# Optimization experiments

Hardware: AMD Instinct MI355X
Metric: run time of the kernel (lower is better)

Reference implementation:

```python
import jax, jax.numpy as jnp
import numpy as np

B, C, S = 16, 128, 32          # batch, in_channel, img_size
HOLE_LO, HOLE_HI = 8, 24       # 16x16 hole where mask==1
HW = S * S
K = HW - (HOLE_HI - HOLE_LO) ** 2   # 768 context (unmasked) pixels per image
EPS = 1e-8                     # torch CosineSimilarity default eps


def setup_inputs() -> dict:
    key = jax.random.key(0)
    ks = jax.random.split(key, 3)
    x = jax.random.normal(ks[0], (B, C, S, S), dtype=jnp.float32)
    # mask: 1 inside the hole, 0 on the context region (fixed K per batch item)
    mask = jnp.zeros((B, 1, S, S), jnp.float32).at[:, :, HOLE_LO:HOLE_HI, HOLE_LO:HOLE_HI].set(1.0)
    # conv_regular_1: Conv2d(img_size**2 -> 256, k=5, pad=2); conv_regular_2: 256 -> 128
    W1 = jax.random.normal(ks[1], (256, HW, 5, 5), jnp.float32) / np.sqrt(HW * 25)
    b1 = jnp.zeros((256,), jnp.float32)
    W2 = jax.random.normal(ks[2], (128, 256, 5, 5), jnp.float32) / np.sqrt(256 * 25)
    b2 = jnp.zeros((128,), jnp.float32)
    return {"x": x, "mask": mask, "W1": W1, "b1": b1, "W2": W2, "b2": b2}


def _conv5x5(x, w, b):
    y = jax.lax.conv_general_dilated(x, w, window_strides=(1, 1),
                                     padding=[(2, 2), (2, 2)],
                                     dimension_numbers=("NCHW", "OIHW", "NCHW"))
    return y + b[None, :, None, None]


def reference(x, mask, W1, b1, W2, b2):
    # context (unmasked) pixel indices, row-major like torch.masked_select
    inv = (1.0 - mask[:, 0]) > 0.5                       # [B,S,S] bool
    idx = jax.vmap(lambda m: jnp.nonzero(m, size=K, fill_value=0)[0])(inv.reshape(B, HW))  # [B,K]
    xf = x.reshape(B, C, HW)                             # [B,C,HW]
    feat = jnp.take_along_axis(xf, idx[:, None, :], axis=2)  # [B,C,K] context features
    # cosine similarity over channel dim WITHOUT materializing [B,C,K,H,W] repeats
    dot = jnp.einsum("bck,bcp->bkp", feat, xf)           # [B,K,HW]
    nf = jnp.maximum(jnp.sqrt(jnp.sum(feat * feat, axis=1)), EPS)  # [B,K]
    nx = jnp.maximum(jnp.sqrt(jnp.sum(xf * xf, axis=1)), EPS)      # [B,HW]
    out = (dot / (nf[:, :, None] * nx[:, None, :])).reshape(B, K, S, S)
    out = out * mask                                     # keep hole region only
    pad = jnp.zeros((B, HW - K, S, S), out.dtype)
    out = jnp.concatenate([out, pad], axis=1)            # [B, HW, S, S]
    out = jax.nn.elu(_conv5x5(out, W1, b1))              # [B,256,S,S]
    out = jax.nn.elu(_conv5x5(out, W2, b2))              # [B,128,S,S]
    return out
```

## Files before the change

kernel.cpp:

```cpp
#include <hip/hip_runtime.h>
#include <hip/hip_fp16.h>
#include <math.h>


#define CC 128
#define HWN 1024
#define KK 768
#define PH 256

typedef _Float16 f16x8 __attribute__((ext_vector_type(8)));
typedef float f32x4 __attribute__((ext_vector_type(4)));

__device__ __forceinline__ int ctx_p(int k) {
    if (k < 256) return k;
    if (k < 512) {
        int r = (k - 256) >> 4, ci = (k - 256) & 15;
        int c = ci < 8 ? ci : ci + 16;
        return (8 + r) * 32 + c;
    }
    return k + 256;
}

__global__ __launch_bounds__(256) void knorm(const float* __restrict__ x, float* __restrict__ rn) {
    int i = blockIdx.x * 256 + threadIdx.x;
    int b = i >> 10, p = i & 1023;
    const float* xp = x + b * CC * HWN + p;
    float ss = 0.f;
#pragma unroll 8
    for (int c = 0; c < CC; ++c) {
        float v = xp[c * HWN];
        ss = fmaf(v, v, ss);
    }
    rn[i] = 1.0f / fmaxf(sqrtf(ss), 1e-8f);
}

__global__ __launch_bounds__(256) void kcos(const float* __restrict__ x, const float* __restrict__ rn,
                                            _Float16* __restrict__ cosT) {
    __shared__ float f[4][CC];
    __shared__ float rf[4];
    const int b = blockIdx.z, g = blockIdx.y;
    const int t = threadIdx.x;
    const int p4 = g * 4;
    for (int s = t; s < 4 * CC; s += 256) {
        int j = s >> 7, c = s & 127;
        int hp = p4 + j;
        f[j][c] = x[(b * CC + c) * HWN + (8 + (hp >> 4)) * 32 + 8 + (hp & 15)];
    }
    if (t < 4) {
        int hp = p4 + t;
        rf[t] = rn[b * HWN + (8 + (hp >> 4)) * 32 + 8 + (hp & 15)];
    }
    __syncthreads();
    const int k = blockIdx.x * 256 + t;
    const int cp = ctx_p(k);
    const float* xp = x + b * CC * HWN + cp;
    float a0 = 0.f, a1 = 0.f, a2 = 0.f, a3 = 0.f;
#pragma unroll 4
    for (int c = 0; c < CC; ++c) {
        float xv = xp[c * HWN];
        a0 = fmaf(f[0][c], xv, a0);
        a1 = fmaf(f[1][c], xv, a1);
        a2 = fmaf(f[2][c], xv, a2);
        a3 = fmaf(f[3][c], xv, a3);
    }
    const float rk = rn[b * HWN + cp];
    _Float16* o = cosT + ((size_t)(b * PH + p4)) * KK + k;
    o[0]          = (_Float16)(a0 * rf[0] * rk);
    o[KK]         = (_Float16)(a1 * rf[1] * rk);
    o[2 * KK]     = (_Float16)(a2 * rf[2] * rk);
    o[3 * KK]     = (_Float16)(a3 * rf[3] * rk);
}

__global__ __launch_bounds__(256) void kprepW1(const float* __restrict__ W1, _Float16* __restrict__ Wh1) {
    const int oc = blockIdx.y;
    const int k = blockIdx.x * 256 + threadIdx.x;
    const float* wp = W1 + ((size_t)oc * HWN + k) * 25;
#pragma unroll
    for (int tap = 0; tap < 25; ++tap)
        Wh1[((size_t)(tap * 256 + oc)) * KK + k] = (_Float16)wp[tap];
}

__global__ __launch_bounds__(256) void kprepW2(const float* __restrict__ W2, _Float16* __restrict__ Wh2) {
    const int oc = blockIdx.x;
    const int ic = threadIdx.x;
    const float* wp = W2 + ((size_t)oc * 256 + ic) * 25;
#pragma unroll
    for (int tap = 0; tap < 25; ++tap)
        Wh2[((size_t)(tap * 128 + oc)) * 256 + ic] = (_Float16)wp[tap];
}

#define C1_MFMA(mi)                                                                          \
    {                                                                                        \
        int pos = pb[mi] + padd;                                                             \
        f16x8 af = *(const f16x8*)(As + pos * 64 + ((kslot ^ (pos & 3)) << 4));              \
        acc[mi][0] = __builtin_amdgcn_mfma_f32_16x16x32_f16(af, bf0, acc[mi][0], 0, 0, 0);   \
        acc[mi][1] = __builtin_amdgcn_mfma_f32_16x16x32_f16(af, bf1, acc[mi][1], 0, 0, 0);   \
    }

__global__ __launch_bounds__(512) void kconv1m(const _Float16* __restrict__ cosT,
                                               const _Float16* __restrict__ Wh1,
                                               float* __restrict__ P) {
    __shared__ __align__(16) char As[576 * 64];
    const int b = blockIdx.z, nq = blockIdx.y, ks = blockIdx.x;
    const int t = threadIdx.x;
    const int lane = t & 63, wid = t >> 6;
    const int mg = wid >> 1, ng = wid & 1;
    const int lm = lane & 15, kslot = lane >> 4;
    const int mbase = (mg == 0) ? 0 : 1 + 6 * mg;
    int pb[7];
#pragma unroll
    for (int mi = 0; mi < 7; ++mi) {
        int p = (mbase + mi) * 16 + lm;
        if (p > 399) p = 399;
        pb[mi] = (p / 20) * 24 + (p % 20);
    }
    const f32x4 zero = {0.f, 0.f, 0.f, 0.f};
    f32x4 acc[7][2];
#pragma unroll
    for (int mi = 0; mi < 7; ++mi) { acc[mi][0] = zero; acc[mi][1] = zero; }

    const int kbeg = ks * 192;
    for (int kc = kbeg; kc < kbeg + 192; kc += 32) {
        __syncthreads();
        for (int s = t; s < 2304; s += 512) {
            int pos = s >> 2, slot = s & 3;
            int pu = pos / 24, pv = pos - pu * 24;
            int4 val = {0, 0, 0, 0};
            if (pu >= 4 && pu < 20 && pv >= 4 && pv < 20) {
                int hp = (pu - 4) * 16 + (pv - 4);
                val = *(const int4*)(cosT + ((size_t)(b * PH + hp)) * KK + kc + slot * 8);
            }
            *(int4*)(As + pos * 64 + ((slot ^ (pos & 3)) << 4)) = val;
        }
        __syncthreads();
        for (int dy = 0; dy < 5; ++dy) {
            for (int dx = 0; dx < 5; ++dx) {
                const int tap = dy * 5 + dx;
                const f16x8 bf0 = *(const f16x8*)(Wh1 + ((size_t)(tap * 256 + nq * 64 + ng * 32 + lm)) * KK + kc + kslot * 8);
                const f16x8 bf1 = *(const f16x8*)(Wh1 + ((size_t)(tap * 256 + nq * 64 + ng * 32 + 16 + lm)) * KK + kc + kslot * 8);
                const int padd = dy * 24 + dx;
#pragma unroll
                for (int mi = 0; mi < 6; ++mi) C1_MFMA(mi)
                if (mg == 0) C1_MFMA(6)
            }
        }
    }
    float* Ps = P + ((size_t)((ks * 16 + b) * 4 + nq)) * 25600;
#pragma unroll
    for (int mi = 0; mi < 7; ++mi) {
        if (mi == 6 && mg != 0) break;
#pragma unroll
        for (int j = 0; j < 2; ++j)
#pragma unroll
            for (int r = 0; r < 4; ++r) {
                int p = (mbase + mi) * 16 + kslot * 4 + r;
                Ps[p * 64 + ng * 32 + j * 16 + lm] = acc[mi][j][r];
            }
    }
}

__global__ __launch_bounds__(256) void kreduce1(const float* __restrict__ P, const float* __restrict__ b1,
                                                _Float16* __restrict__ Y1T) {
    int i = blockIdx.x * 256 + threadIdx.x;
    int ocl = i & 63;
    int nq = (i >> 6) & 3;
    int bp = i >> 8;
    int p = bp % 400, b = bp / 400;
    float s = 0.f;
#pragma unroll
    for (int ks = 0; ks < 4; ++ks)
        s += P[((size_t)((ks * 16 + b) * 4 + nq)) * 25600 + p * 64 + ocl];
    int oc = nq * 64 + ocl;
    float y = s + b1[oc];
    y = y > 0.f ? y : expm1f(y);
    Y1T[((size_t)(b * 400 + p)) * 256 + oc] = (_Float16)y;
}

__global__ __launch_bounds__(512) void kconv2m(const _Float16* __restrict__ Y1T,
                                               const _Float16* __restrict__ Wh2,
                                               float* __restrict__ P) {
    __shared__ __align__(16) char As[784 * 64];
    const int b = blockIdx.z, mh = blockIdx.y, ks = blockIdx.x;
    const int t = threadIdx.x;
    const int lane = t & 63, wid = t >> 6;
    const int mg = wid >> 2, ng = wid & 3;
    const int lm = lane & 15, kslot = lane >> 4;
    const int ic0 = ks * 32;
    for (int s = t; s < 3136; s += 512) {
        int pos = s >> 2, slot = s & 3;
        int r = pos / 28, c = pos - r * 28;
        int4 val = {0, 0, 0, 0};
        if (r >= 4 && r < 24 && c >= 4 && c < 24)
            val = *(const int4*)(Y1T + ((size_t)(b * 400 + (r - 4) * 20 + (c - 4))) * 256 + ic0 + slot * 8);
        *(int4*)(As + pos * 64 + ((slot ^ (pos & 3)) << 4)) = val;
    }
    int pbs[9];
#pragma unroll
    for (int mi = 0; mi < 9; ++mi) {
        int p = (mh * 18 + mg * 9 + mi) * 16 + lm;
        pbs[mi] = (p / 24) * 28 + (p % 24);
    }
    const f32x4 zero = {0.f, 0.f, 0.f, 0.f};
    f32x4 acc[9][2];
#pragma unroll
    for (int mi = 0; mi < 9; ++mi) { acc[mi][0] = zero; acc[mi][1] = zero; }
    __syncthreads();
    for (int dy = 0; dy < 5; ++dy) {
        for (int dx = 0; dx < 5; ++dx) {
            const int tap = dy * 5 + dx;
            const f16x8 bf0 = *(const f16x8*)(Wh2 + ((size_t)(tap * 128 + ng * 32 + lm)) * 256 + ic0 + kslot * 8);
            const f16x8 bf1 = *(const f16x8*)(Wh2 + ((size_t)(tap * 128 + ng * 32 + 16 + lm)) * 256 + ic0 + kslot * 8);
            const int padd = dy * 28 + dx;
#pragma unroll
            for (int mi = 0; mi < 9; ++mi) {
                int pos = pbs[mi] + padd;
                f16x8 af = *(const f16x8*)(As + pos * 64 + ((kslot ^ (pos & 3)) << 4));
                acc[mi][0] = __builtin_amdgcn_mfma_f32_16x16x32_f16(af, bf0, acc[mi][0], 0, 0, 0);
                acc[mi][1] = __builtin_amdgcn_mfma_f32_16x16x32_f16(af, bf1, acc[mi][1], 0, 0, 0);
            }
        }
    }
    float* Ps = P + ((size_t)((ks * 16 + b) * 2 + mh)) * 36864;
#pragma unroll
    for (int mi = 0; mi < 9; ++mi)
#pragma unroll
        for (int j = 0; j < 2; ++j)
#pragma unroll
            for (int r = 0; r < 4; ++r) {
                int p = (mg * 9 + mi) * 16 + kslot * 4 + r;
                Ps[p * 128 + ng * 32 + j * 16 + lm] = acc[mi][j][r];
            }
}

__global__ __launch_bounds__(256) void kreduce2(const float* __restrict__ P, const float* __restrict__ b2,
                                                float* __restrict__ out) {
    int i = blockIdx.x * 256 + threadIdx.x;
    int oc = i & 127;
    int p = (i >> 7) % 576;
    int b = (i >> 7) / 576;
    int mh = p >= 288 ? 1 : 0;
    int pl = p - mh * 288;
    float s = 0.f;
#pragma unroll
    for (int ks = 0; ks < 8; ++ks)
        s += P[((size_t)((ks * 16 + b) * 2 + mh)) * 36864 + pl * 128 + oc];
    float y = s + b2[oc];
    y = y > 0.f ? y : expm1f(y);
    int ou = p / 24, ov = p - ou * 24;
    out[((size_t)(b * 128 + oc)) * 1024 + (4 + ou) * 32 + 4 + ov] = y;
}

extern "C" void kernel_launch(void* const* d_in, const int* in_sizes, int n_in,
                              void* d_out, int out_size, void* d_ws, size_t ws_size,
                              hipStream_t stream) {
    const float* x  = (const float*)d_in[0];
    const float* W1 = (const float*)d_in[2];
    const float* b1 = (const float*)d_in[3];
    const float* W2 = (const float*)d_in[4];
    const float* b2 = (const float*)d_in[5];
    float* out = (float*)d_out;

    char* ws = (char*)d_ws;
    float*    rn   = (float*)(ws + 0);
    _Float16* cosT = (_Float16*)(ws + 65536);
    _Float16* Wh1  = (_Float16*)(ws + 6356992);
    _Float16* Wh2  = (_Float16*)(ws + 16187392);
    _Float16* Y1T  = (_Float16*)(ws + 17825792);
    float*    P    = (float*)(ws + 21102592);

    hipMemsetAsync(d_out, 0, (size_t)out_size * sizeof(float), stream);

    knorm<<<64, 256, 0, stream>>>(x, rn);
    kcos<<<dim3(3, 64, 16), 256, 0, stream>>>(x, rn, cosT);
    kprepW1<<<dim3(3, 256), 256, 0, stream>>>(W1, Wh1);
    kprepW2<<<128, 256, 0, stream>>>(W2, Wh2);
    kconv1m<<<dim3(4, 4, 16), 512, 0, stream>>>(cosT, Wh1, P);
    kreduce1<<<6400, 256, 0, stream>>>(P, b1, Y1T);
    kconv2m<<<dim3(8, 2, 16), 512, 0, stream>>>(Y1T, Wh2, P);
    kreduce2<<<4608, 256, 0, stream>>>(P, b2, out);
}
```

Baseline: 266.6 us.

## Retile conv MFMA kernels for more blocks and smaller per-warp tiles

Both implicit-GEMM conv kernels now split the output pixels across more blocks. Conv1 goes from 4 to 8 y-blocks (2 output-channel halves by 4 pixel groups), and conv2 goes from 2 to 4 pixel groups. Each warp now holds 2-3 pixel tiles by 64 output channels instead of 7-9 tiles by 32, which cuts register pressure and raises occupancy, with launch_bounds(512,4) set to match. The shared-memory A tile changes from an XOR-swizzled layout to planar per-kslot layout, and the P partial buffers and reduce kernels are re-indexed to the new layout. The two weight-prep kernels are merged into one launch. The trade-off is more reloading of weights and the A halo per output, in exchange for better parallelism.

```diff
diff --git a/kernel.cpp b/kernel.cpp
--- a/kernel.cpp
+++ b/kernel.cpp
@@ -71,53 +71,61 @@
     o[3 * KK]     = (_Float16)(a3 * rf[3] * rk);
 }
 
-__global__ __launch_bounds__(256) void kprepW1(const float* __restrict__ W1, _Float16* __restrict__ Wh1) {
-    const int oc = blockIdx.y;
-    const int k = blockIdx.x * 256 + threadIdx.x;
-    const float* wp = W1 + ((size_t)oc * HWN + k) * 25;
-#pragma unroll
-    for (int tap = 0; tap < 25; ++tap)
-        Wh1[((size_t)(tap * 256 + oc)) * KK + k] = (_Float16)wp[tap];
-}
-
-__global__ __launch_bounds__(256) void kprepW2(const float* __restrict__ W2, _Float16* __restrict__ Wh2) {
-    const int oc = blockIdx.x;
-    const int ic = threadIdx.x;
-    const float* wp = W2 + ((size_t)oc * 256 + ic) * 25;
-#pragma unroll
-    for (int tap = 0; tap < 25; ++tap)
-        Wh2[((size_t)(tap * 128 + oc)) * 256 + ic] = (_Float16)wp[tap];
-}
-
-#define C1_MFMA(mi)                                                                          \
-    {                                                                                        \
-        int pos = pb[mi] + padd;                                                             \
-        f16x8 af = *(const f16x8*)(As + pos * 64 + ((kslot ^ (pos & 3)) << 4));              \
-        acc[mi][0] = __builtin_amdgcn_mfma_f32_16x16x32_f16(af, bf0, acc[mi][0], 0, 0, 0);   \
-        acc[mi][1] = __builtin_amdgcn_mfma_f32_16x16x32_f16(af, bf1, acc[mi][1], 0, 0, 0);   \
-    }
-
-__global__ __launch_bounds__(512) void kconv1m(const _Float16* __restrict__ cosT,
-                                               const _Float16* __restrict__ Wh1,
-                                               float* __restrict__ P) {
-    __shared__ __align__(16) char As[576 * 64];
-    const int b = blockIdx.z, nq = blockIdx.y, ks = blockIdx.x;
+__global__ __launch_bounds__(256) void kprepW(const float* __restrict__ W1, const float* __restrict__ W2,
+                                              _Float16* __restrict__ Wh1, _Float16* __restrict__ Wh2) {
+    const int bid = blockIdx.x;
+    if (bid < 768) {
+        const int oc = bid & 255, kch = bid >> 8;
+        const int k = kch * 256 + threadIdx.x;
+        const float* wp = W1 + ((size_t)oc * HWN + k) * 25;
+#pragma unroll
+        for (int tap = 0; tap < 25; ++tap)
+            Wh1[((size_t)(tap * 256 + oc)) * KK + k] = (_Float16)wp[tap];
+    } else {
+        const int oc = bid - 768;
+        const int ic = threadIdx.x;
+        const float* wp = W2 + ((size_t)oc * 256 + ic) * 25;
+#pragma unroll
+        for (int tap = 0; tap < 25; ++tap)
+            Wh2[((size_t)(tap * 128 + oc)) * 256 + ic] = (_Float16)wp[tap];
+    }
+}
+
+__constant__ int c1_mhs[4] = {0, 7, 13, 19};
+__constant__ int c1_mhc[4] = {7, 6, 6, 6};
+__constant__ int c1_off7[4] = {0, 2, 4, 6};
+__constant__ int c1_cnt7[4] = {2, 2, 2, 1};
+__constant__ int c1_off6[4] = {0, 2, 4, 5};
+__constant__ int c1_cnt6[4] = {2, 2, 1, 1};
+
+__global__ __launch_bounds__(512, 4) void kconv1m(const _Float16* __restrict__ cosT,
+                                                  const _Float16* __restrict__ Wh1,
+                                                  float* __restrict__ P) {
+    __shared__ __align__(16) char As[4 * 578 * 16];
+    const int b = blockIdx.z, ks = blockIdx.x;
+    const int nq = blockIdx.y >> 2, mh = blockIdx.y & 3;
     const int t = threadIdx.x;
     const int lane = t & 63, wid = t >> 6;
     const int mg = wid >> 1, ng = wid & 1;
     const int lm = lane & 15, kslot = lane >> 4;
-    const int mbase = (mg == 0) ? 0 : 1 + 6 * mg;
-    int pb[7];
-#pragma unroll
-    for (int mi = 0; mi < 7; ++mi) {
-        int p = (mbase + mi) * 16 + lm;
+    const int mhc = c1_mhc[mh];
+    const int tile0 = c1_mhs[mh] + (mhc == 7 ? c1_off7[mg] : c1_off6[mg]);
+    const int cnt = (mhc == 7 ? c1_cnt7[mg] : c1_cnt6[mg]);
+    int pb[2];
+#pragma unroll
+    for (int mi = 0; mi < 2; ++mi) {
+        int p = (tile0 + mi) * 16 + lm;
         if (p > 399) p = 399;
         pb[mi] = (p / 20) * 24 + (p % 20);
     }
     const f32x4 zero = {0.f, 0.f, 0.f, 0.f};
-    f32x4 acc[7][2];
-#pragma unroll
-    for (int mi = 0; mi < 7; ++mi) { acc[mi][0] = zero; acc[mi][1] = zero; }
+    f32x4 acc[2][4];
+#pragma unroll
+    for (int mi = 0; mi < 2; ++mi)
+#pragma unroll
+        for (int j = 0; j < 4; ++j) acc[mi][j] = zero;
+
+    const _Float16* Wb = Wh1 + (size_t)(nq * 128 + ng * 64 + lm) * KK + kslot * 8;
 
     const int kbeg = ks * 192;
     for (int kc = kbeg; kc < kbeg + 192; kc += 32) {
@@ -130,60 +138,75 @@
                 int hp = (pu - 4) * 16 + (pv - 4);
                 val = *(const int4*)(cosT + ((size_t)(b * PH + hp)) * KK + kc + slot * 8);
             }
-            *(int4*)(As + pos * 64 + ((slot ^ (pos & 3)) << 4)) = val;
+            *(int4*)(As + (slot * 578 + pos) * 16) = val;
         }
         __syncthreads();
         for (int dy = 0; dy < 5; ++dy) {
+#pragma unroll
             for (int dx = 0; dx < 5; ++dx) {
                 const int tap = dy * 5 + dx;
-                const f16x8 bf0 = *(const f16x8*)(Wh1 + ((size_t)(tap * 256 + nq * 64 + ng * 32 + lm)) * KK + kc + kslot * 8);
-                const f16x8 bf1 = *(const f16x8*)(Wh1 + ((size_t)(tap * 256 + nq * 64 + ng * 32 + 16 + lm)) * KK + kc + kslot * 8);
+                const _Float16* wt = Wb + (size_t)tap * (256 * KK) + kc;
+                const f16x8 bf0 = *(const f16x8*)(wt);
+                const f16x8 bf1 = *(const f16x8*)(wt + 16 * KK);
+                const f16x8 bf2 = *(const f16x8*)(wt + 32 * KK);
+                const f16x8 bf3 = *(const f16x8*)(wt + 48 * KK);
                 const int padd = dy * 24 + dx;
 #pragma unroll
-                for (int mi = 0; mi < 6; ++mi) C1_MFMA(mi)
-                if (mg == 0) C1_MFMA(6)
+                for (int mi = 0; mi < 2; ++mi) {
+                    if (mi < cnt) {
+                        f16x8 af = *(const f16x8*)(As + (kslot * 578 + pb[mi] + padd) * 16);
+                        acc[mi][0] = __builtin_amdgcn_mfma_f32_16x16x32_f16(af, bf0, acc[mi][0], 0, 0, 0);
+                        acc[mi][1] = __builtin_amdgcn_mfma_f32_16x16x32_f16(af, bf1, acc[mi][1], 0, 0, 0);
+                        acc[mi][2] = __builtin_amdgcn_mfma_f32_16x16x32_f16(af, bf2, acc[mi][2], 0, 0, 0);
+                        acc[mi][3] = __builtin_amdgcn_mfma_f32_16x16x32_f16(af, bf3, acc[mi][3], 0, 0, 0);
+                    }
+                }
             }
         }
     }
-    float* Ps = P + ((size_t)((ks * 16 + b) * 4 + nq)) * 25600;
-#pragma unroll
-    for (int mi = 0; mi < 7; ++mi) {
-        if (mi == 6 && mg != 0) break;
-#pragma unroll
-        for (int j = 0; j < 2; ++j)
-#pragma unroll
-            for (int r = 0; r < 4; ++r) {
-                int p = (mbase + mi) * 16 + kslot * 4 + r;
-                Ps[p * 64 + ng * 32 + j * 16 + lm] = acc[mi][j][r];
-            }
+    float* Ps = P + ((size_t)((ks * 16 + b) * 2 + nq)) * 51200;
+#pragma unroll
+    for (int mi = 0; mi < 2; ++mi) {
+        if (mi < cnt) {
+#pragma unroll
+            for (int j = 0; j < 4; ++j)
+#pragma unroll
+                for (int r = 0; r < 4; ++r) {
+                    int p = (tile0 + mi) * 16 + kslot * 4 + r;
+                    Ps[p * 128 + ng * 64 + j * 16 + lm] = acc[mi][j][r];
+                }
+        }
     }
 }
 
 __global__ __launch_bounds__(256) void kreduce1(const float* __restrict__ P, const float* __restrict__ b1,
                                                 _Float16* __restrict__ Y1T) {
     int i = blockIdx.x * 256 + threadIdx.x;
-    int ocl = i & 63;
-    int nq = (i >> 6) & 3;
+    int ocl = i & 127;
+    int nq = (i >> 7) & 1;
     int bp = i >> 8;
     int p = bp % 400, b = bp / 400;
     float s = 0.f;
 #pragma unroll
     for (int ks = 0; ks < 4; ++ks)
-        s += P[((size_t)((ks * 16 + b) * 4 + nq)) * 25600 + p * 64 + ocl];
-    int oc = nq * 64 + ocl;
+        s += P[((size_t)((ks * 16 + b) * 2 + nq)) * 51200 + p * 128 + ocl];
+    int oc = nq * 128 + ocl;
     float y = s + b1[oc];
     y = y > 0.f ? y : expm1f(y);
     Y1T[((size_t)(b * 400 + p)) * 256 + oc] = (_Float16)y;
 }
 
-__global__ __launch_bounds__(512) void kconv2m(const _Float16* __restrict__ Y1T,
-                                               const _Float16* __restrict__ Wh2,
-                                               float* __restrict__ P) {
-    __shared__ __align__(16) char As[784 * 64];
+__constant__ int c2_off[4] = {0, 3, 5, 7};
+__constant__ int c2_cnt[4] = {3, 2, 2, 2};
+
+__global__ __launch_bounds__(512, 4) void kconv2m(const _Float16* __restrict__ Y1T,
+                                                  const _Float16* __restrict__ Wh2,
+                                                  float* __restrict__ P) {
+    __shared__ __align__(16) char As[4 * 786 * 16];
     const int b = blockIdx.z, mh = blockIdx.y, ks = blockIdx.x;
     const int t = threadIdx.x;
     const int lane = t & 63, wid = t >> 6;
-    const int mg = wid >> 2, ng = wid & 3;
+    const int mg = wid >> 1, ng = wid & 1;
     const int lm = lane & 15, kslot = lane >> 4;
     const int ic0 = ks * 32;
     for (int s = t; s < 3136; s += 512) {
@@ -192,44 +215,60 @@
         int4 val = {0, 0, 0, 0};
         if (r >= 4 && r < 24 && c >= 4 && c < 24)
             val = *(const int4*)(Y1T + ((size_t)(b * 400 + (r - 4) * 20 + (c - 4))) * 256 + ic0 + slot * 8);
-        *(int4*)(As + pos * 64 + ((slot ^ (pos & 3)) << 4)) = val;
-    }
-    int pbs[9];
-#pragma unroll
-    for (int mi = 0; mi < 9; ++mi) {
-        int p = (mh * 18 + mg * 9 + mi) * 16 + lm;
-        pbs[mi] = (p / 24) * 28 + (p % 24);
+        *(int4*)(As + (slot * 786 + pos) * 16) = val;
+    }
+    const int tile0 = mh * 9 + c2_off[mg];
+    const int cnt = c2_cnt[mg];
+    int pb[3];
+#pragma unroll
+    for (int mi = 0; mi < 3; ++mi) {
+        int p = (tile0 + mi) * 16 + lm;
+        if (p > 575) p = 575;
+        pb[mi] = (p / 24) * 28 + (p % 24);
     }
     const f32x4 zero = {0.f, 0.f, 0.f, 0.f};
-    f32x4 acc[9][2];
-#pragma unroll
-    for (int mi = 0; mi < 9; ++mi) { acc[mi][0] = zero; acc[mi][1] = zero; }
+    f32x4 acc[3][4];
+#pragma unroll
+    for (int mi = 0; mi < 3; ++mi)
+#pragma unroll
+        for (int j = 0; j < 4; ++j) acc[mi][j] = zero;
+    const _Float16* Wb = Wh2 + (size_t)(ng * 64 + lm) * 256 + ic0 + kslot * 8;
     __syncthreads();
     for (int dy = 0; dy < 5; ++dy) {
+#pragma unroll
         for (int dx = 0; dx < 5; ++dx) {
             const int tap = dy * 5 + dx;
-            const f16x8 bf0 = *(const f16x8*)(Wh2 + ((size_t)(tap * 128 + ng * 32 + lm)) * 256 + ic0 + kslot * 8);
-            const f16x8 bf1 = *(const f16x8*)(Wh2 + ((size_t)(tap * 128 + ng * 32 + 16 + lm)) * 256 + ic0 + kslot * 8);
+            const _Float16* wt = Wb + (size_t)tap * (128 * 256);
+            const f16x8 bf0 = *(const f16x8*)(wt);
+            const f16x8 bf1 = *(const f16x8*)(wt + 16 * 256);
+            const f16x8 bf2 = *(const f16x8*)(wt + 32 * 256);
+            const f16x8 bf3 = *(const f16x8*)(wt + 48 * 256);
             const int padd = dy * 28 + dx;
 #pragma unroll
-            for (int mi = 0; mi < 9; ++mi) {
-                int pos = pbs[mi] + padd;
-                f16x8 af = *(const f16x8*)(As + pos * 64 + ((kslot ^ (pos & 3)) << 4));
-                acc[mi][0] = __builtin_amdgcn_mfma_f32_16x16x32_f16(af, bf0, acc[mi][0], 0, 0, 0);
-                acc[mi][1] = __builtin_amdgcn_mfma_f32_16x16x32_f16(af, bf1, acc[mi][1], 0, 0, 0);
+            for (int mi = 0; mi < 3; ++mi) {
+                if (mi < cnt) {
+                    f16x8 af = *(const f16x8*)(As + (kslot * 786 + pb[mi] + padd) * 16);
+                    acc[mi][0] = __builtin_amdgcn_mfma_f32_16x16x32_f16(af, bf0, acc[mi][0], 0, 0, 0);
+                    acc[mi][1] = __builtin_amdgcn_mfma_f32_16x16x32_f16(af, bf1, acc[mi][1], 0, 0, 0);
+                    acc[mi][2] = __builtin_amdgcn_mfma_f32_16x16x32_f16(af, bf2, acc[mi][2], 0, 0, 0);
+                    acc[mi][3] = __builtin_amdgcn_mfma_f32_16x16x32_f16(af, bf3, acc[mi][3], 0, 0, 0);
+                }
             }
         }
     }
-    float* Ps = P + ((size_t)((ks * 16 + b) * 2 + mh)) * 36864;
-#pragma unroll
-    for (int mi = 0; mi < 9; ++mi)
-#pragma unroll
-        for (int j = 0; j < 2; ++j)
-#pragma unroll
-            for (int r = 0; r < 4; ++r) {
-                int p = (mg * 9 + mi) * 16 + kslot * 4 + r;
-                Ps[p * 128 + ng * 32 + j * 16 + lm] = acc[mi][j][r];
-            }
+    float* Ps = P + ((size_t)(ks * 16 + b)) * 73728;
+#pragma unroll
+    for (int mi = 0; mi < 3; ++mi) {
+        if (mi < cnt) {
+#pragma unroll
+            for (int j = 0; j < 4; ++j)
+#pragma unroll
+                for (int r = 0; r < 4; ++r) {
+                    int p = (tile0 + mi) * 16 + kslot * 4 + r;
+                    Ps[p * 128 + ng * 64 + j * 16 + lm] = acc[mi][j][r];
+                }
+        }
+    }
 }
 
 __global__ __launch_bounds__(256) void kreduce2(const float* __restrict__ P, const float* __restrict__ b2,
@@ -238,12 +277,10 @@
     int oc = i & 127;
     int p = (i >> 7) % 576;
     int b = (i >> 7) / 576;
-    int mh = p >= 288 ? 1 : 0;
-    int pl = p - mh * 288;
     float s = 0.f;
 #pragma unroll
     for (int ks = 0; ks < 8; ++ks)
-        s += P[((size_t)((ks * 16 + b) * 2 + mh)) * 36864 + pl * 128 + oc];
+        s += P[((size_t)(ks * 16 + b)) * 73728 + p * 128 + oc];
     float y = s + b2[oc];
     y = y > 0.f ? y : expm1f(y);
     int ou = p / 24, ov = p - ou * 24;
@@ -272,10 +309,9 @@
 
     knorm<<<64, 256, 0, stream>>>(x, rn);
     kcos<<<dim3(3, 64, 16), 256, 0, stream>>>(x, rn, cosT);
-    kprepW1<<<dim3(3, 256), 256, 0, stream>>>(W1, Wh1);
-    kprepW2<<<128, 256, 0, stream>>>(W2, Wh2);
-    kconv1m<<<dim3(4, 4, 16), 512, 0, stream>>>(cosT, Wh1, P);
+    kprepW<<<896, 256, 0, stream>>>(W1, W2, Wh1, Wh2);
+    kconv1m<<<dim3(4, 8, 16), 512, 0, stream>>>(cosT, Wh1, P);
     kreduce1<<<6400, 256, 0, stream>>>(P, b1, Y1T);
-    kconv2m<<<dim3(8, 2, 16), 512, 0, stream>>>(Y1T, Wh2, P);
+    kconv2m<<<dim3(8, 4, 16), 512, 0, stream>>>(Y1T, Wh2, P);
     kreduce2<<<4608, 256, 0, stream>>>(P, b2, out);
 }
```

Result: slower. 476.7 us (+78.8%).
